# Performance work log

Measured on AMD Instinct MI355X. Metric: run time of the kernel, lower is better.

The kernel has to match this reference:

```python
import jax, jax.numpy as jnp
import numpy as np

R_SCALES = (1, 2, 4, 10, 25)
DIM = 300
B, L = 64, 800


def setup_inputs() -> dict:
    key = jax.random.key(0)
    k1, k2, k3 = jax.random.split(key, 3)
    inputs_c_e = jax.random.normal(k1, (B, L, DIM), dtype=jnp.float32)
    # xavier-normal-ish weights for the 5 per-scale Linear(DIM, DIM) layers
    std = float(np.sqrt(2.0 / (DIM + DIM)))
    W = jax.random.normal(k2, (5, DIM, DIM), dtype=jnp.float32) * std
    b = jax.random.normal(k3, (5, DIM), dtype=jnp.float32) * 0.01
    return {"inputs_c_e": inputs_c_e, "W": W, "b": b}


def _one_scale(x, W, bias, r):
    # x: [B, L, D]; W: [D, D] (torch Linear weight, y = x @ W.T + b)
    Bn, Ln, D = x.shape
    g = Ln // r
    rest = Ln - g * r
    # segment sum over groups of size r  -> [B, g, D]
    seg = x[:, : g * r].reshape(Bn, g, r, D).sum(axis=2)
    y = jax.nn.relu(jnp.einsum('bgd,ed->bge', seg, W) + bias) / r  # [B, g, D]
    y = jnp.repeat(y, r, axis=1)  # broadcast back to [B, g*r, D]
    if rest != 0:
        s = x[:, g * r:].sum(axis=1) * (r / rest)  # [B, D]
        yr = jax.nn.relu(s @ W.T + bias) / r       # [B, D]
        yr = jnp.broadcast_to(yr[:, None, :], (Bn, rest, D))
        y = jnp.concatenate([y, yr], axis=1)
    return y  # [B, L, D]


def reference(inputs_c_e, W, b):
    outs = [_one_scale(inputs_c_e, W[n], b[n], r) for n, r in enumerate(R_SCALES)]
    return jnp.stack(outs, axis=0)  # [5, B, L, D]
```

## Files before the change

kernel.cpp:

```cpp
#include <hip/hip_runtime.h>


typedef short bf16x8 __attribute__((ext_vector_type(8)));
typedef float f32x4  __attribute__((ext_vector_type(4)));

namespace {
constexpr int D    = 300;
constexpr int LSEQ = 800;
constexpr int KP   = 320;
constexpr int NP   = 320;
constexpr int CSTR = 308;
constexpr int SMEM_BYTES = 32 * CSTR * 4;
}

__device__ __forceinline__ unsigned short f2bf(float f) {
  unsigned u = __float_as_uint(f);
  u += 0x7fffu + ((u >> 16) & 1u);
  return (unsigned short)(u >> 16);
}

__global__ __launch_bounds__(256)
void convert_w(const float* __restrict__ W, short* __restrict__ Wb) {
  const int item = blockIdx.x * 256 + threadIdx.x;
  if (item >= 5 * NP * KP / 8) return;
  const int off = item * 8;
  const int n   = off / (NP * KP);
  const int rem = off - n * (NP * KP);
  const int c   = rem / KP;
  const int k0  = rem - c * KP;
  float s[8];
  #pragma unroll
  for (int j = 0; j < 8; ++j) s[j] = 0.f;
  if (c < D) {
    const float* wp = W + (size_t)n * D * D + (size_t)c * D + k0;
    if (k0 < 296) {
      const float4 v0 = *(const float4*)(wp);
      const float4 v1 = *(const float4*)(wp + 4);
      s[0] = v0.x; s[1] = v0.y; s[2] = v0.z; s[3] = v0.w;
      s[4] = v1.x; s[5] = v1.y; s[6] = v1.z; s[7] = v1.w;
    } else if (k0 == 296) {
      const float4 v0 = *(const float4*)(wp);
      s[0] = v0.x; s[1] = v0.y; s[2] = v0.z; s[3] = v0.w;
    }
  }
  bf16x8 p;
  #pragma unroll
  for (int j = 0; j < 8; ++j) p[j] = (short)f2bf(s[j]);
  *(bf16x8*)(Wb + (size_t)off) = p;
}

template<int N, int R, int G>
__device__ __forceinline__ void ce_body(const int tile, char* __restrict__ smem,
    const float* __restrict__ x, const short* __restrict__ Wb,
    const float* __restrict__ bias, float* __restrict__ out) {
  const int tid = threadIdx.x;
  const int m0  = tile * 32;
  constexpr int BQ = (R <= 5) ? R : 5;

  #pragma unroll
  for (int it = 0; it < 5; ++it) {
    const int cidx = tid + it * 256;
    const int row  = cidx / 40;
    const int k0   = (cidx - row * 40) * 8;
    float s[8];
    #pragma unroll
    for (int j = 0; j < 8; ++j) s[j] = 0.f;
    if (k0 < D) {
      const int m   = m0 + row;
      const int bb  = m / G;
      const int grp = m - bb * G;
      const float* xp = x + ((size_t)(bb * LSEQ + grp * R)) * D + k0;
      if (k0 <= D - 8) {
        for (int qb = 0; qb < R; qb += BQ) {
          float4 a0[BQ], a1[BQ];
          #pragma unroll
          for (int j = 0; j < BQ; ++j) {
            a0[j] = *(const float4*)(xp + (size_t)(qb + j) * D);
            a1[j] = *(const float4*)(xp + (size_t)(qb + j) * D + 4);
          }
          #pragma unroll
          for (int j = 0; j < BQ; ++j) {
            s[0] += a0[j].x; s[1] += a0[j].y; s[2] += a0[j].z; s[3] += a0[j].w;
            s[4] += a1[j].x; s[5] += a1[j].y; s[6] += a1[j].z; s[7] += a1[j].w;
          }
        }
      } else {
        for (int qb = 0; qb < R; qb += BQ) {
          float4 a0[BQ];
          #pragma unroll
          for (int j = 0; j < BQ; ++j)
            a0[j] = *(const float4*)(xp + (size_t)(qb + j) * D);
          #pragma unroll
          for (int j = 0; j < BQ; ++j) {
            s[0] += a0[j].x; s[1] += a0[j].y; s[2] += a0[j].z; s[3] += a0[j].w;
          }
        }
      }
    }
    bf16x8 p;
    #pragma unroll
    for (int j = 0; j < 8; ++j) p[j] = (short)f2bf(s[j]);
    const int boff = (row * 640 + k0 * 2) ^ ((row & 7) << 4);
    *(bf16x8*)(smem + boff) = p;
  }

  const int wv   = tid >> 6;
  const int lane = tid & 63;
  const int cr   = lane & 15;
  const int kh   = lane >> 4;

  const short* __restrict__ Wn = Wb + (size_t)N * NP * KP;
  const short* __restrict__ wp[5];
  #pragma unroll
  for (int t = 0; t < 5; ++t)
    wp[t] = Wn + (size_t)((wv * 5 + t) * 16 + cr) * KP + kh * 8;

  bf16x8 bpre[5];
  #pragma unroll
  for (int t = 0; t < 5; ++t) bpre[t] = *(const bf16x8*)(wp[t]);

  __syncthreads();

  f32x4 acc[2][5];
  #pragma unroll
  for (int mt = 0; mt < 2; ++mt)
    #pragma unroll
    for (int t = 0; t < 5; ++t) acc[mt][t] = (f32x4){0.f, 0.f, 0.f, 0.f};

  const int swz0 = (cr & 7) << 4;
  const int abase0 = cr * 640        + kh * 16;
  const int abase1 = (16 + cr) * 640 + kh * 16;

  bf16x8 a0pre = *(const bf16x8*)(smem + (abase0 ^ swz0));
  bf16x8 a1pre = *(const bf16x8*)(smem + (abase1 ^ swz0));

  #pragma unroll
  for (int ks = 0; ks < 10; ++ks) {
    bf16x8 bcur[5];
    #pragma unroll
    for (int t = 0; t < 5; ++t) bcur[t] = bpre[t];
    const bf16x8 a0 = a0pre, a1 = a1pre;
    if (ks < 9) {
      #pragma unroll
      for (int t = 0; t < 5; ++t) bpre[t] = *(const bf16x8*)(wp[t] + (ks + 1) * 32);
      a0pre = *(const bf16x8*)(smem + ((abase0 + (ks + 1) * 64) ^ swz0));
      a1pre = *(const bf16x8*)(smem + ((abase1 + (ks + 1) * 64) ^ swz0));
    }
    #pragma unroll
    for (int t = 0; t < 5; ++t) {
      acc[0][t] = __builtin_amdgcn_mfma_f32_16x16x32_bf16(a0, bcur[t], acc[0][t], 0, 0, 0);
      acc[1][t] = __builtin_amdgcn_mfma_f32_16x16x32_bf16(a1, bcur[t], acc[1][t], 0, 0, 0);
    }
  }
  __syncthreads();

  float* __restrict__ cout = (float*)smem;
  const float inv_r = 1.0f / (float)R;
  #pragma unroll
  for (int t = 0; t < 5; ++t) {
    const int col = (wv * 5 + t) * 16 + cr;
    if (col < D) {
      const float bv = bias[N * D + col];
      #pragma unroll
      for (int mt = 0; mt < 2; ++mt)
        #pragma unroll
        for (int j = 0; j < 4; ++j) {
          const int row = mt * 16 + kh * 4 + j;
          cout[row * CSTR + col] = fmaxf(acc[mt][t][j] + bv, 0.f) * inv_r;
        }
    }
  }
  __syncthreads();

  constexpr int TOTAL = 32 * R * 75;
  for (int i = tid; i < TOTAL; i += 256) {
    const int rowrep = i / 75;
    const int chunk  = i - rowrep * 75;
    const int ml     = rowrep / R;
    const int q      = rowrep - ml * R;
    const int m      = m0 + ml;
    const int bb     = m / G;
    const int grp    = m - bb * G;
    const f32x4 v = *(const f32x4*)(cout + ml * CSTR + chunk * 4);
    float* __restrict__ op =
        out + ((size_t)((N * 64 + bb) * LSEQ) + grp * R + q) * D + chunk * 4;
    __builtin_nontemporal_store(v, (f32x4*)op);
  }
}

__global__ __launch_bounds__(256, 4)
void ce_mfma10(const float* __restrict__ x, const short* __restrict__ Wb,
               const float* __restrict__ bias, float* __restrict__ out) {
  __shared__ __align__(16) char smem[SMEM_BYTES];
  const int bid = blockIdx.x;
  if (bid < 64)        ce_body<4, 25, 32 >(bid,        smem, x, Wb, bias, out);
  else if (bid < 224)  ce_body<3, 10, 80 >(bid - 64,   smem, x, Wb, bias, out);
  else if (bid < 624)  ce_body<2, 4, 200 >(bid - 224,  smem, x, Wb, bias, out);
  else if (bid < 1424) ce_body<1, 2, 400 >(bid - 624,  smem, x, Wb, bias, out);
  else                 ce_body<0, 1, 800 >(bid - 1424, smem, x, Wb, bias, out);
}

extern "C" void kernel_launch(void* const* d_in, const int* in_sizes, int n_in,
                              void* d_out, int out_size, void* d_ws, size_t ws_size,
                              hipStream_t stream) {
  const float* x    = (const float*)d_in[0];
  const float* W    = (const float*)d_in[1];
  const float* bias = (const float*)d_in[2];
  float* out        = (float*)d_out;
  short* Wb         = (short*)d_ws;

  convert_w<<<250, 256, 0, stream>>>(W, Wb);
  ce_mfma10<<<3024, 256, 0, stream>>>(x, Wb, bias, out);
}
```

Before: 145.5 us.

## Split compute and broadcast into compact bf16 intermediate plus expand kernel

The GEMM kernel now writes one bf16 row per group into workspace, and a separate expand kernel broadcasts each row to all repeated positions of the fp32 output. The aim is to separate the write-bound broadcast from the MFMA compute so each kernel has an even, streaming write pattern. It adds an extra launch and an intermediate round trip, and it rounds the output to bf16 precision. A fallback path keeps the old fused kernel, now with plain stores, for small workspaces.

```diff
diff --git a/kernel.cpp b/kernel.cpp
--- a/kernel.cpp
+++ b/kernel.cpp
@@ -2,6 +2,7 @@
 
 
 typedef short bf16x8 __attribute__((ext_vector_type(8)));
+typedef short bf16x4 __attribute__((ext_vector_type(4)));
 typedef float f32x4  __attribute__((ext_vector_type(4)));
 
 namespace {
@@ -10,7 +11,12 @@
 constexpr int KP   = 320;
 constexpr int NP   = 320;
 constexpr int CSTR = 308;
+constexpr int YSTR = 304;
 constexpr int SMEM_BYTES = 32 * CSTR * 4;
+constexpr size_t WB_SHORTS = (size_t)5 * NP * KP;
+constexpr int YB0 = 0, YB1 = 51200, YB2 = 76800, YB3 = 89600, YB4 = 94720;
+constexpr int YROWS = 96768;
+constexpr size_t WS_NEEDED = (WB_SHORTS + (size_t)YROWS * YSTR) * 2;
 }
 
 __device__ __forceinline__ unsigned short f2bf(float f) {
@@ -49,10 +55,11 @@
   *(bf16x8*)(Wb + (size_t)off) = p;
 }
 
-template<int N, int R, int G>
+
+template<int N, int R, int G, int YB>
 __device__ __forceinline__ void ce_body(const int tile, char* __restrict__ smem,
     const float* __restrict__ x, const short* __restrict__ Wb,
-    const float* __restrict__ bias, float* __restrict__ out) {
+    const float* __restrict__ bias, short* __restrict__ y) {
   const int tid = threadIdx.x;
   const int m0  = tile * 32;
   constexpr int BQ = (R <= 5) ? R : 5;
@@ -172,6 +179,176 @@
   }
   __syncthreads();
 
+  for (int i = tid; i < 32 * 75; i += 256) {
+    const int ml = i / 75;
+    const int c4 = i - ml * 75;
+    const f32x4 v = *(const f32x4*)(cout + ml * CSTR + c4 * 4);
+    bf16x4 p;
+    p[0] = (short)f2bf(v[0]); p[1] = (short)f2bf(v[1]);
+    p[2] = (short)f2bf(v[2]); p[3] = (short)f2bf(v[3]);
+    *(bf16x4*)(y + (size_t)(YB + m0 + ml) * YSTR + c4 * 4) = p;
+  }
+}
+
+__global__ __launch_bounds__(256, 4)
+void ce_y(const float* __restrict__ x, const short* __restrict__ Wb,
+          const float* __restrict__ bias, short* __restrict__ y) {
+  __shared__ __align__(16) char smem[SMEM_BYTES];
+  const int bid = blockIdx.x;
+  if (bid < 64)        ce_body<4, 25, 32 , YB4>(bid,        smem, x, Wb, bias, y);
+  else if (bid < 224)  ce_body<3, 10, 80 , YB3>(bid - 64,   smem, x, Wb, bias, y);
+  else if (bid < 624)  ce_body<2, 4, 200 , YB2>(bid - 224,  smem, x, Wb, bias, y);
+  else if (bid < 1424) ce_body<1, 2, 400 , YB1>(bid - 624,  smem, x, Wb, bias, y);
+  else                 ce_body<0, 1, 800 , YB0>(bid - 1424, smem, x, Wb, bias, y);
+}
+
+
+template<int N, int R, int YB>
+__device__ __forceinline__ void expand_scale(const short* __restrict__ y,
+    float* __restrict__ out, const int bloc, const int nblocks) {
+  constexpr int ITEMS = 64 * LSEQ * 75;
+  for (int i = bloc * 256 + (int)threadIdx.x; i < ITEMS; i += nblocks * 256) {
+    const int row = i / 75;
+    const int c4  = i - row * 75;
+    const int b   = row / LSEQ;
+    const int l   = row - b * LSEQ;
+    const int g   = l / R;
+    const bf16x4 sv =
+        *(const bf16x4*)(y + (size_t)(YB + b * (LSEQ / R) + g) * YSTR + c4 * 4);
+    f32x4 v;
+    v[0] = __uint_as_float(((unsigned)(unsigned short)sv[0]) << 16);
+    v[1] = __uint_as_float(((unsigned)(unsigned short)sv[1]) << 16);
+    v[2] = __uint_as_float(((unsigned)(unsigned short)sv[2]) << 16);
+    v[3] = __uint_as_float(((unsigned)(unsigned short)sv[3]) << 16);
+    *(f32x4*)(out + ((size_t)(N * 64 + b) * LSEQ + l) * D + c4 * 4) = v;
+  }
+}
+
+__global__ __launch_bounds__(256)
+void expand(const short* __restrict__ y, float* __restrict__ out) {
+  constexpr int BPS = 410;
+  const int s    = blockIdx.x / BPS;
+  const int bloc = blockIdx.x - s * BPS;
+  if (s == 0)      expand_scale<0, 1 , YB0>(y, out, bloc, BPS);
+  else if (s == 1) expand_scale<1, 2 , YB1>(y, out, bloc, BPS);
+  else if (s == 2) expand_scale<2, 4 , YB2>(y, out, bloc, BPS);
+  else if (s == 3) expand_scale<3, 10, YB3>(y, out, bloc, BPS);
+  else             expand_scale<4, 25, YB4>(y, out, bloc, BPS);
+}
+
+
+template<int N, int R, int G>
+__device__ __forceinline__ void ce_body_fb(const int tile, char* __restrict__ smem,
+    const float* __restrict__ x, const short* __restrict__ Wb,
+    const float* __restrict__ bias, float* __restrict__ out) {
+  const int tid = threadIdx.x;
+  const int m0  = tile * 32;
+  constexpr int BQ = (R <= 5) ? R : 5;
+  #pragma unroll
+  for (int it = 0; it < 5; ++it) {
+    const int cidx = tid + it * 256;
+    const int row  = cidx / 40;
+    const int k0   = (cidx - row * 40) * 8;
+    float s[8];
+    #pragma unroll
+    for (int j = 0; j < 8; ++j) s[j] = 0.f;
+    if (k0 < D) {
+      const int m   = m0 + row;
+      const int bb  = m / G;
+      const int grp = m - bb * G;
+      const float* xp = x + ((size_t)(bb * LSEQ + grp * R)) * D + k0;
+      if (k0 <= D - 8) {
+        for (int qb = 0; qb < R; qb += BQ) {
+          float4 a0[BQ], a1[BQ];
+          #pragma unroll
+          for (int j = 0; j < BQ; ++j) {
+            a0[j] = *(const float4*)(xp + (size_t)(qb + j) * D);
+            a1[j] = *(const float4*)(xp + (size_t)(qb + j) * D + 4);
+          }
+          #pragma unroll
+          for (int j = 0; j < BQ; ++j) {
+            s[0] += a0[j].x; s[1] += a0[j].y; s[2] += a0[j].z; s[3] += a0[j].w;
+            s[4] += a1[j].x; s[5] += a1[j].y; s[6] += a1[j].z; s[7] += a1[j].w;
+          }
+        }
+      } else {
+        for (int qb = 0; qb < R; qb += BQ) {
+          float4 a0[BQ];
+          #pragma unroll
+          for (int j = 0; j < BQ; ++j)
+            a0[j] = *(const float4*)(xp + (size_t)(qb + j) * D);
+          #pragma unroll
+          for (int j = 0; j < BQ; ++j) {
+            s[0] += a0[j].x; s[1] += a0[j].y; s[2] += a0[j].z; s[3] += a0[j].w;
+          }
+        }
+      }
+    }
+    bf16x8 p;
+    #pragma unroll
+    for (int j = 0; j < 8; ++j) p[j] = (short)f2bf(s[j]);
+    const int boff = (row * 640 + k0 * 2) ^ ((row & 7) << 4);
+    *(bf16x8*)(smem + boff) = p;
+  }
+  const int wv   = tid >> 6;
+  const int lane = tid & 63;
+  const int cr   = lane & 15;
+  const int kh   = lane >> 4;
+  const short* __restrict__ Wn = Wb + (size_t)N * NP * KP;
+  const short* __restrict__ wp[5];
+  #pragma unroll
+  for (int t = 0; t < 5; ++t)
+    wp[t] = Wn + (size_t)((wv * 5 + t) * 16 + cr) * KP + kh * 8;
+  bf16x8 bpre[5];
+  #pragma unroll
+  for (int t = 0; t < 5; ++t) bpre[t] = *(const bf16x8*)(wp[t]);
+  __syncthreads();
+  f32x4 acc[2][5];
+  #pragma unroll
+  for (int mt = 0; mt < 2; ++mt)
+    #pragma unroll
+    for (int t = 0; t < 5; ++t) acc[mt][t] = (f32x4){0.f, 0.f, 0.f, 0.f};
+  const int swz0 = (cr & 7) << 4;
+  const int abase0 = cr * 640        + kh * 16;
+  const int abase1 = (16 + cr) * 640 + kh * 16;
+  bf16x8 a0pre = *(const bf16x8*)(smem + (abase0 ^ swz0));
+  bf16x8 a1pre = *(const bf16x8*)(smem + (abase1 ^ swz0));
+  #pragma unroll
+  for (int ks = 0; ks < 10; ++ks) {
+    bf16x8 bcur[5];
+    #pragma unroll
+    for (int t = 0; t < 5; ++t) bcur[t] = bpre[t];
+    const bf16x8 a0 = a0pre, a1 = a1pre;
+    if (ks < 9) {
+      #pragma unroll
+      for (int t = 0; t < 5; ++t) bpre[t] = *(const bf16x8*)(wp[t] + (ks + 1) * 32);
+      a0pre = *(const bf16x8*)(smem + ((abase0 + (ks + 1) * 64) ^ swz0));
+      a1pre = *(const bf16x8*)(smem + ((abase1 + (ks + 1) * 64) ^ swz0));
+    }
+    #pragma unroll
+    for (int t = 0; t < 5; ++t) {
+      acc[0][t] = __builtin_amdgcn_mfma_f32_16x16x32_bf16(a0, bcur[t], acc[0][t], 0, 0, 0);
+      acc[1][t] = __builtin_amdgcn_mfma_f32_16x16x32_bf16(a1, bcur[t], acc[1][t], 0, 0, 0);
+    }
+  }
+  __syncthreads();
+  float* __restrict__ cout = (float*)smem;
+  const float inv_r = 1.0f / (float)R;
+  #pragma unroll
+  for (int t = 0; t < 5; ++t) {
+    const int col = (wv * 5 + t) * 16 + cr;
+    if (col < D) {
+      const float bv = bias[N * D + col];
+      #pragma unroll
+      for (int mt = 0; mt < 2; ++mt)
+        #pragma unroll
+        for (int j = 0; j < 4; ++j) {
+          const int row = mt * 16 + kh * 4 + j;
+          cout[row * CSTR + col] = fmaxf(acc[mt][t][j] + bv, 0.f) * inv_r;
+        }
+    }
+  }
+  __syncthreads();
   constexpr int TOTAL = 32 * R * 75;
   for (int i = tid; i < TOTAL; i += 256) {
     const int rowrep = i / 75;
@@ -184,20 +361,20 @@
     const f32x4 v = *(const f32x4*)(cout + ml * CSTR + chunk * 4);
     float* __restrict__ op =
         out + ((size_t)((N * 64 + bb) * LSEQ) + grp * R + q) * D + chunk * 4;
-    __builtin_nontemporal_store(v, (f32x4*)op);
+    *(f32x4*)op = v;
   }
 }
 
 __global__ __launch_bounds__(256, 4)
-void ce_mfma10(const float* __restrict__ x, const short* __restrict__ Wb,
-               const float* __restrict__ bias, float* __restrict__ out) {
+void ce_mfma_fb(const float* __restrict__ x, const short* __restrict__ Wb,
+                const float* __restrict__ bias, float* __restrict__ out) {
   __shared__ __align__(16) char smem[SMEM_BYTES];
   const int bid = blockIdx.x;
-  if (bid < 64)        ce_body<4, 25, 32 >(bid,        smem, x, Wb, bias, out);
-  else if (bid < 224)  ce_body<3, 10, 80 >(bid - 64,   smem, x, Wb, bias, out);
-  else if (bid < 624)  ce_body<2, 4, 200 >(bid - 224,  smem, x, Wb, bias, out);
-  else if (bid < 1424) ce_body<1, 2, 400 >(bid - 624,  smem, x, Wb, bias, out);
-  else                 ce_body<0, 1, 800 >(bid - 1424, smem, x, Wb, bias, out);
+  if (bid < 64)        ce_body_fb<4, 25, 32 >(bid,        smem, x, Wb, bias, out);
+  else if (bid < 224)  ce_body_fb<3, 10, 80 >(bid - 64,   smem, x, Wb, bias, out);
+  else if (bid < 624)  ce_body_fb<2, 4, 200 >(bid - 224,  smem, x, Wb, bias, out);
+  else if (bid < 1424) ce_body_fb<1, 2, 400 >(bid - 624,  smem, x, Wb, bias, out);
+  else                 ce_body_fb<0, 1, 800 >(bid - 1424, smem, x, Wb, bias, out);
 }
 
 extern "C" void kernel_launch(void* const* d_in, const int* in_sizes, int n_in,
@@ -207,8 +384,14 @@
   const float* W    = (const float*)d_in[1];
   const float* bias = (const float*)d_in[2];
   float* out        = (float*)d_out;
-  short* Wb         = (short*)d_ws;
-
-  convert_w<<<250, 256, 0, stream>>>(W, Wb);
-  ce_mfma10<<<3024, 256, 0, stream>>>(x, Wb, bias, out);
-}
+  short* ws         = (short*)d_ws;
+
+  convert_w<<<250, 256, 0, stream>>>(W, ws);
+  if (ws_size >= WS_NEEDED) {
+    short* y = ws + WB_SHORTS;
+    ce_y<<<3024, 256, 0, stream>>>(x, ws, bias, y);
+    expand<<<2050, 256, 0, stream>>>(y, out);
+  } else {
+    ce_mfma_fb<<<3024, 256, 0, stream>>>(x, ws, bias, out);
+  }
+}
```

New measurement: 188.4 us. 29.5% more time.

## Persist blocks over multiple tiles for r=1,2 with double-buffered staging

Applied to the files above, without the earlier changes.

For the two smallest scales, each block now handles four 32-row tiles. It issues the global loads for the next tile's segment sums into registers while running MFMA on the current tile, with double-buffered LDS staging. The output staging tile is now stored in bf16 instead of fp32, which halves LDS use. Output stores become plain stores instead of nontemporal ones. Launch bounds drop from 4 to 2 blocks per CU and the grid shrinks. The change adds register pressure from up to 5*R float4 prefetch arrays, lowers occupancy, and rounds the output to bf16 precision.

```diff
diff --git a/kernel.cpp b/kernel.cpp
--- a/kernel.cpp
+++ b/kernel.cpp
@@ -2,6 +2,7 @@
 
 
 typedef short bf16x8 __attribute__((ext_vector_type(8)));
+typedef short bf16x4 __attribute__((ext_vector_type(4)));
 typedef float f32x4  __attribute__((ext_vector_type(4)));
 
 namespace {
@@ -9,14 +10,18 @@
 constexpr int LSEQ = 800;
 constexpr int KP   = 320;
 constexpr int NP   = 320;
-constexpr int CSTR = 308;
-constexpr int SMEM_BYTES = 32 * CSTR * 4;
+constexpr int CB   = 308;
+constexpr int BUF  = 20480;
+constexpr int SMEM_BYTES = 2 * BUF;
 }
 
 __device__ __forceinline__ unsigned short f2bf(float f) {
   unsigned u = __float_as_uint(f);
   u += 0x7fffu + ((u >> 16) & 1u);
   return (unsigned short)(u >> 16);
+}
+__device__ __forceinline__ float bf2f(short s) {
+  return __uint_as_float(((unsigned)(unsigned short)s) << 16);
 }
 
 __global__ __launch_bounds__(256)
@@ -49,8 +54,194 @@
   *(bf16x8*)(Wb + (size_t)off) = p;
 }
 
+
 template<int N, int R, int G>
-__device__ __forceinline__ void ce_body(const int tile, char* __restrict__ smem,
+__device__ __forceinline__ void store_expanded(const short* __restrict__ cout,
+    const int m0, float* __restrict__ out) {
+  const int tid = threadIdx.x;
+  constexpr int TOTAL = 32 * R * 75;
+  for (int i = tid; i < TOTAL; i += 256) {
+    const int rowrep = i / 75;
+    const int chunk  = i - rowrep * 75;
+    const int ml     = rowrep / R;
+    const int q      = rowrep - ml * R;
+    const int m      = m0 + ml;
+    const int bb     = m / G;
+    const int grp    = m - bb * G;
+    const bf16x4 sv = *(const bf16x4*)(cout + ml * CB + chunk * 4);
+    f32x4 v;
+    v[0] = bf2f(sv[0]); v[1] = bf2f(sv[1]); v[2] = bf2f(sv[2]); v[3] = bf2f(sv[3]);
+    float* __restrict__ op =
+        out + ((size_t)((N * 64 + bb) * LSEQ) + grp * R + q) * D + chunk * 4;
+    *(f32x4*)op = v;
+  }
+}
+
+template<int N>
+__device__ __forceinline__ void mfma_tile(const char* __restrict__ smem,
+    const short* __restrict__ wp[5], f32x4 acc[2][5]) {
+  const int lane = threadIdx.x & 63;
+  const int cr   = lane & 15;
+  const int kh   = lane >> 4;
+  const int swz0 = (cr & 7) << 4;
+  const int abase0 = cr * 640        + kh * 16;
+  const int abase1 = (16 + cr) * 640 + kh * 16;
+
+  bf16x8 bpre[5];
+  #pragma unroll
+  for (int t = 0; t < 5; ++t) bpre[t] = *(const bf16x8*)(wp[t]);
+  bf16x8 a0pre = *(const bf16x8*)(smem + (abase0 ^ swz0));
+  bf16x8 a1pre = *(const bf16x8*)(smem + (abase1 ^ swz0));
+
+  #pragma unroll
+  for (int ks = 0; ks < 10; ++ks) {
+    bf16x8 bcur[5];
+    #pragma unroll
+    for (int t = 0; t < 5; ++t) bcur[t] = bpre[t];
+    const bf16x8 a0 = a0pre, a1 = a1pre;
+    if (ks < 9) {
+      #pragma unroll
+      for (int t = 0; t < 5; ++t) bpre[t] = *(const bf16x8*)(wp[t] + (ks + 1) * 32);
+      a0pre = *(const bf16x8*)(smem + ((abase0 + (ks + 1) * 64) ^ swz0));
+      a1pre = *(const bf16x8*)(smem + ((abase1 + (ks + 1) * 64) ^ swz0));
+    }
+    #pragma unroll
+    for (int t = 0; t < 5; ++t) {
+      acc[0][t] = __builtin_amdgcn_mfma_f32_16x16x32_bf16(a0, bcur[t], acc[0][t], 0, 0, 0);
+      acc[1][t] = __builtin_amdgcn_mfma_f32_16x16x32_bf16(a1, bcur[t], acc[1][t], 0, 0, 0);
+    }
+  }
+}
+
+template<int N, int R>
+__device__ __forceinline__ void write_cout(short* __restrict__ cout,
+    f32x4 acc[2][5], const float bv[5]) {
+  const int lane = threadIdx.x & 63;
+  const int wv   = threadIdx.x >> 6;
+  const int cr   = lane & 15;
+  const int kh   = lane >> 4;
+  const float inv_r = 1.0f / (float)R;
+  #pragma unroll
+  for (int t = 0; t < 5; ++t) {
+    const int col = (wv * 5 + t) * 16 + cr;
+    if (col < D) {
+      #pragma unroll
+      for (int mt = 0; mt < 2; ++mt)
+        #pragma unroll
+        for (int j = 0; j < 4; ++j) {
+          const int row = mt * 16 + kh * 4 + j;
+          cout[row * CB + col] =
+              (short)f2bf(fmaxf(acc[mt][t][j] + bv[t], 0.f) * inv_r);
+        }
+    }
+  }
+}
+
+
+template<int N, int R, int G, int TPB>
+__device__ __forceinline__ void ce_persist(const int base, char* __restrict__ smem,
+    const float* __restrict__ x, const short* __restrict__ Wb,
+    const float* __restrict__ bias, float* __restrict__ out) {
+  const int tid  = threadIdx.x;
+  const int wv   = tid >> 6;
+  const int lane = tid & 63;
+  const int cr   = lane & 15;
+  const int kh   = lane >> 4;
+
+  const short* __restrict__ Wn = Wb + (size_t)N * NP * KP;
+  const short* __restrict__ wp[5];
+  #pragma unroll
+  for (int t = 0; t < 5; ++t)
+    wp[t] = Wn + (size_t)((wv * 5 + t) * 16 + cr) * KP + kh * 8;
+  float bv[5];
+  #pragma unroll
+  for (int t = 0; t < 5; ++t) {
+    const int col = (wv * 5 + t) * 16 + cr;
+    bv[t] = (col < D) ? bias[N * D + col] : 0.f;
+  }
+
+  float4 v0[5 * R], v1[5 * R];
+  int srow[5], sk0[5];
+  #pragma unroll
+  for (int it = 0; it < 5; ++it) {
+    const int cidx = tid + it * 256;
+    srow[it] = cidx / 40;
+    sk0[it]  = (cidx - srow[it] * 40) * 8;
+  }
+
+  auto stage_issue = [&](int m0) {
+    #pragma unroll
+    for (int it = 0; it < 5; ++it) {
+      const int k0 = sk0[it];
+      if (k0 < D) {
+        const int m   = m0 + srow[it];
+        const int bb  = m / G;
+        const int grp = m - bb * G;
+        const float* xp = x + ((size_t)(bb * LSEQ + grp * R)) * D + k0;
+        #pragma unroll
+        for (int q = 0; q < R; ++q) {
+          v0[it * R + q] = *(const float4*)(xp + (size_t)q * D);
+          v1[it * R + q] = (k0 < 296) ? *(const float4*)(xp + (size_t)q * D + 4)
+                                      : (float4){0.f, 0.f, 0.f, 0.f};
+        }
+      }
+    }
+  };
+  auto stage_consume = [&](char* buf) {
+    #pragma unroll
+    for (int it = 0; it < 5; ++it) {
+      const int k0  = sk0[it];
+      const int row = srow[it];
+      float s[8];
+      #pragma unroll
+      for (int j = 0; j < 8; ++j) s[j] = 0.f;
+      if (k0 < D) {
+        #pragma unroll
+        for (int q = 0; q < R; ++q) {
+          s[0] += v0[it * R + q].x; s[1] += v0[it * R + q].y;
+          s[2] += v0[it * R + q].z; s[3] += v0[it * R + q].w;
+          s[4] += v1[it * R + q].x; s[5] += v1[it * R + q].y;
+          s[6] += v1[it * R + q].z; s[7] += v1[it * R + q].w;
+        }
+      }
+      bf16x8 p;
+      #pragma unroll
+      for (int j = 0; j < 8; ++j) p[j] = (short)f2bf(s[j]);
+      const int boff = (row * 640 + k0 * 2) ^ ((row & 7) << 4);
+      *(bf16x8*)(buf + boff) = p;
+    }
+  };
+
+  stage_issue(base * TPB * 32);
+  stage_consume(smem);
+  __syncthreads();
+
+  for (int t = 0; t < TPB; ++t) {
+    char* curb = smem + (t & 1) * BUF;
+    char* nxtb = smem + ((t + 1) & 1) * BUF;
+    const int m0 = (base * TPB + t) * 32;
+
+    if (t + 1 < TPB) stage_issue((base * TPB + t + 1) * 32);
+
+    f32x4 acc[2][5];
+    #pragma unroll
+    for (int mt = 0; mt < 2; ++mt)
+      #pragma unroll
+      for (int tt = 0; tt < 5; ++tt) acc[mt][tt] = (f32x4){0.f, 0.f, 0.f, 0.f};
+    mfma_tile<N>(curb, wp, acc);
+
+    __syncthreads();
+    if (t + 1 < TPB) stage_consume(nxtb);
+    write_cout<N, R>((short*)curb, acc, bv);
+    __syncthreads();
+
+    store_expanded<N, R, G>((const short*)curb, m0, out);
+  }
+}
+
+
+template<int N, int R, int G>
+__device__ __forceinline__ void ce_classic(const int tile, char* __restrict__ smem,
     const float* __restrict__ x, const short* __restrict__ Wb,
     const float* __restrict__ bias, float* __restrict__ out) {
   const int tid = threadIdx.x;
@@ -108,96 +299,44 @@
   const int lane = tid & 63;
   const int cr   = lane & 15;
   const int kh   = lane >> 4;
-
   const short* __restrict__ Wn = Wb + (size_t)N * NP * KP;
   const short* __restrict__ wp[5];
   #pragma unroll
   for (int t = 0; t < 5; ++t)
     wp[t] = Wn + (size_t)((wv * 5 + t) * 16 + cr) * KP + kh * 8;
-
-  bf16x8 bpre[5];
-  #pragma unroll
-  for (int t = 0; t < 5; ++t) bpre[t] = *(const bf16x8*)(wp[t]);
-
-  __syncthreads();
-
-  f32x4 acc[2][5];
-  #pragma unroll
-  for (int mt = 0; mt < 2; ++mt)
-    #pragma unroll
-    for (int t = 0; t < 5; ++t) acc[mt][t] = (f32x4){0.f, 0.f, 0.f, 0.f};
-
-  const int swz0 = (cr & 7) << 4;
-  const int abase0 = cr * 640        + kh * 16;
-  const int abase1 = (16 + cr) * 640 + kh * 16;
-
-  bf16x8 a0pre = *(const bf16x8*)(smem + (abase0 ^ swz0));
-  bf16x8 a1pre = *(const bf16x8*)(smem + (abase1 ^ swz0));
-
-  #pragma unroll
-  for (int ks = 0; ks < 10; ++ks) {
-    bf16x8 bcur[5];
-    #pragma unroll
-    for (int t = 0; t < 5; ++t) bcur[t] = bpre[t];
-    const bf16x8 a0 = a0pre, a1 = a1pre;
-    if (ks < 9) {
-      #pragma unroll
-      for (int t = 0; t < 5; ++t) bpre[t] = *(const bf16x8*)(wp[t] + (ks + 1) * 32);
-      a0pre = *(const bf16x8*)(smem + ((abase0 + (ks + 1) * 64) ^ swz0));
-      a1pre = *(const bf16x8*)(smem + ((abase1 + (ks + 1) * 64) ^ swz0));
-    }
-    #pragma unroll
-    for (int t = 0; t < 5; ++t) {
-      acc[0][t] = __builtin_amdgcn_mfma_f32_16x16x32_bf16(a0, bcur[t], acc[0][t], 0, 0, 0);
-      acc[1][t] = __builtin_amdgcn_mfma_f32_16x16x32_bf16(a1, bcur[t], acc[1][t], 0, 0, 0);
-    }
-  }
-  __syncthreads();
-
-  float* __restrict__ cout = (float*)smem;
-  const float inv_r = 1.0f / (float)R;
+  float bv[5];
   #pragma unroll
   for (int t = 0; t < 5; ++t) {
     const int col = (wv * 5 + t) * 16 + cr;
-    if (col < D) {
-      const float bv = bias[N * D + col];
-      #pragma unroll
-      for (int mt = 0; mt < 2; ++mt)
-        #pragma unroll
-        for (int j = 0; j < 4; ++j) {
-          const int row = mt * 16 + kh * 4 + j;
-          cout[row * CSTR + col] = fmaxf(acc[mt][t][j] + bv, 0.f) * inv_r;
-        }
-    }
+    bv[t] = (col < D) ? bias[N * D + col] : 0.f;
   }
   __syncthreads();
 
-  constexpr int TOTAL = 32 * R * 75;
-  for (int i = tid; i < TOTAL; i += 256) {
-    const int rowrep = i / 75;
-    const int chunk  = i - rowrep * 75;
-    const int ml     = rowrep / R;
-    const int q      = rowrep - ml * R;
-    const int m      = m0 + ml;
-    const int bb     = m / G;
-    const int grp    = m - bb * G;
-    const f32x4 v = *(const f32x4*)(cout + ml * CSTR + chunk * 4);
-    float* __restrict__ op =
-        out + ((size_t)((N * 64 + bb) * LSEQ) + grp * R + q) * D + chunk * 4;
-    __builtin_nontemporal_store(v, (f32x4*)op);
-  }
-}
-
-__global__ __launch_bounds__(256, 4)
-void ce_mfma10(const float* __restrict__ x, const short* __restrict__ Wb,
+  f32x4 acc[2][5];
+  #pragma unroll
+  for (int mt = 0; mt < 2; ++mt)
+    #pragma unroll
+    for (int t = 0; t < 5; ++t) acc[mt][t] = (f32x4){0.f, 0.f, 0.f, 0.f};
+  mfma_tile<N>(smem, wp, acc);
+  __syncthreads();
+
+  short* cout = (short*)(smem + BUF);
+  write_cout<N, R>(cout, acc, bv);
+  __syncthreads();
+
+  store_expanded<N, R, G>(cout, m0, out);
+}
+
+__global__ __launch_bounds__(256, 2)
+void ce_mfma12(const float* __restrict__ x, const short* __restrict__ Wb,
                const float* __restrict__ bias, float* __restrict__ out) {
   __shared__ __align__(16) char smem[SMEM_BYTES];
   const int bid = blockIdx.x;
-  if (bid < 64)        ce_body<4, 25, 32 >(bid,        smem, x, Wb, bias, out);
-  else if (bid < 224)  ce_body<3, 10, 80 >(bid - 64,   smem, x, Wb, bias, out);
-  else if (bid < 624)  ce_body<2, 4, 200 >(bid - 224,  smem, x, Wb, bias, out);
-  else if (bid < 1424) ce_body<1, 2, 400 >(bid - 624,  smem, x, Wb, bias, out);
-  else                 ce_body<0, 1, 800 >(bid - 1424, smem, x, Wb, bias, out);
+  if (bid < 64)        ce_classic<4, 25, 32 >(bid,        smem, x, Wb, bias, out);
+  else if (bid < 224)  ce_classic<3, 10, 80 >(bid - 64,   smem, x, Wb, bias, out);
+  else if (bid < 624)  ce_classic<2, 4, 200 >(bid - 224,  smem, x, Wb, bias, out);
+  else if (bid < 824)  ce_persist<1, 2, 400, 4>(bid - 624, smem, x, Wb, bias, out);
+  else                 ce_persist<0, 1, 800, 4>(bid - 824, smem, x, Wb, bias, out);
 }
 
 extern "C" void kernel_launch(void* const* d_in, const int* in_sizes, int n_in,
@@ -210,5 +349,5 @@
   short* Wb         = (short*)d_ws;
 
   convert_w<<<250, 256, 0, stream>>>(W, Wb);
-  ce_mfma10<<<3024, 256, 0, stream>>>(x, Wb, bias, out);
-}
+  ce_mfma12<<<1224, 256, 0, stream>>>(x, Wb, bias, out);
+}
```

Measured after the change: 229.1 us. 57.5% more time.
